# Optimization experiments

Measured on AMD Instinct MI355X. Metric: run time of the kernel, lower is better.

The kernel has to match this reference:

```python
import jax, jax.numpy as jnp
import numpy as np

B, S, H, E, V = 4, 256, 1024, 1024, 50257
PAD = 0
DOM = 0.9   # skipLayersDominance
EPS = 1e-5  # LayerNorm eps (torch default)


def setup_inputs() -> dict:
    key = jax.random.key(0)
    ks = jax.random.split(key, 6)
    emb = jax.random.normal(ks[0], (V, E), jnp.float32) * 0.02
    emb = emb.at[PAD].set(0.0)  # padding_idx row zeroed like nn.Embedding
    labels = jax.random.randint(ks[1], (B, S), 0, V)
    W_in = jax.random.normal(ks[2], (E, H), jnp.float32) * (1.0 / np.sqrt(E))
    b_in = jnp.zeros((H,), jnp.float32)
    # Conv1d(2H, H, kernel_size=1, groups=H) weight -> [H, 2] (per-head pair mix)
    W_sani = jax.random.normal(ks[3], (H, 2), jnp.float32) * (1.0 / np.sqrt(2.0))
    b_sani = jnp.zeros((H,), jnp.float32)
    ln_w = jnp.ones((H,), jnp.float32)
    ln_b = jnp.zeros((H,), jnp.float32)
    W_out = jax.random.normal(ks[4], (H, E), jnp.float32) * (1.0 / np.sqrt(H))
    b_out = jnp.zeros((E,), jnp.float32)
    return dict(labels=labels, emb=emb, W_in=W_in, b_in=b_in, W_sani=W_sani,
                b_sani=b_sani, ln_w=ln_w, ln_b=ln_b, W_out=W_out, b_out=b_out)


def _layernorm(x, w, b):
    mu = x.mean(-1, keepdims=True)
    var = x.var(-1, keepdims=True)
    return (x - mu) * jax.lax.rsqrt(var + EPS) * w + b


def _forward(labels, emb, W_in, b_in, W_sani, b_sani, ln_w, ln_b, W_out, b_out):
    x = emb[labels]                                # [B,S,E] inputsEmbeddings
    h = jax.nn.relu(x @ W_in + b_in)               # [B,S,H] inputState
    pos = jnp.arange(S)

    def step(hidden, L):
        # positions <= L are replaced by blank (zeros) per the torch cat logic
        mask = (pos > L)[None, :, None]
        shifted = jnp.concatenate([jnp.zeros_like(hidden[:, :1]), hidden[:, :-1]], axis=1)
        prev = jnp.where(mask, shifted, 0.0)       # hidden[t-1] for t>L else 0
        curr = jnp.where(mask, hidden, 0.0)        # hidden[t]   for t>L else 0
        # torch stack(dim=1)+reshape(B, 2H, 1) == concat(prev, curr) on features;
        # grouped conv (groups=H, 2 ch/group, k=1): out[g] = W[g,0]*cat[2g] + W[g,1]*cat[2g+1] + b[g]
        pair = jnp.concatenate([prev, curr], axis=-1).reshape(B, S, H, 2)
        out = jax.nn.relu(jnp.einsum('bshc,hc->bsh', pair, W_sani) + b_sani)
        out = out * (1.0 - DOM) + hidden           # skipLayers: + sequentialInputState
        out = _layernorm(out, ln_w, ln_b)           # skipLayersNorm
        return out, None

    h, _ = jax.lax.scan(jax.checkpoint(step), h, jnp.arange(S))
    y = jax.nn.relu(h @ W_out + b_out)             # [B,S,E]
    # torch CrossEntropyLoss with float (soft) targets: classes along dim=1 (S)
    logp = jax.nn.log_softmax(y, axis=1)
    loss = -(x * logp).sum(axis=1).mean()
    return loss


def reference(labels, emb, W_in, b_in, W_sani, b_sani, ln_w, ln_b, W_out, b_out):
    return _forward(labels, emb, W_in, b_in, W_sani, b_sani, ln_w, ln_b, W_out, b_out)
```

## Files before the change

kernel.cpp:

```cpp
#include <hip/hip_runtime.h>
#include <cstdint>

#define H_DIM 1024
#define S_LEN 256
#define NBLK_SCAN 128
#define GDEPTH 16
#define DOMC ((float)(1.0 - 0.9))
#define EPS_LN 1e-5f

typedef float v2f __attribute__((ext_vector_type(2)));

template <int CTRL, int RMASK, bool BC>
__device__ __forceinline__ float dpp_term(float x) {
    return __int_as_float(__builtin_amdgcn_update_dpp(
        0, __float_as_int(x), CTRL, RMASK, 0xf, BC));
}
__device__ __forceinline__ float wave_reduce_sum(float x) {
    x += dpp_term<0x111, 0xf, true>(x);
    x += dpp_term<0x112, 0xf, true>(x);
    x += dpp_term<0x114, 0xf, true>(x);
    x += dpp_term<0x118, 0xf, true>(x);
    x += dpp_term<0x142, 0xa, false>(x);
    x += dpp_term<0x143, 0xc, false>(x);
    return __int_as_float(__builtin_amdgcn_readlane(__float_as_int(x), 63));
}

__device__ __forceinline__ void lds_release_fence() {
    asm volatile("s_waitcnt lgkmcnt(0)" ::: "memory");
}

__device__ __forceinline__ int llc_load_int(const int* p) {
    int v;
    asm volatile("global_load_dword %0, %1, off sc0 sc1\n\ts_waitcnt vmcnt(0)"
                 : "=v"(v) : "v"(p) : "memory");
    return v;
}
__device__ __forceinline__ void llc_store_int(int* p, int v) {
    asm volatile("global_store_dword %0, %1, off sc0 sc1" :: "v"(p), "v"(v)
                 : "memory");
}
__device__ __forceinline__ void llc_store_row_nowait(float* base, const float* h) {
    asm volatile(
        "global_store_dword %16, %0, off sc0 sc1\n\t"
        "global_store_dword %16, %1, off offset:256 sc0 sc1\n\t"
        "global_store_dword %16, %2, off offset:512 sc0 sc1\n\t"
        "global_store_dword %16, %3, off offset:768 sc0 sc1\n\t"
        "global_store_dword %16, %4, off offset:1024 sc0 sc1\n\t"
        "global_store_dword %16, %5, off offset:1280 sc0 sc1\n\t"
        "global_store_dword %16, %6, off offset:1536 sc0 sc1\n\t"
        "global_store_dword %16, %7, off offset:1792 sc0 sc1\n\t"
        "global_store_dword %16, %8, off offset:2048 sc0 sc1\n\t"
        "global_store_dword %16, %9, off offset:2304 sc0 sc1\n\t"
        "global_store_dword %16, %10, off offset:2560 sc0 sc1\n\t"
        "global_store_dword %16, %11, off offset:2816 sc0 sc1\n\t"
        "global_store_dword %16, %12, off offset:3072 sc0 sc1\n\t"
        "global_store_dword %16, %13, off offset:3328 sc0 sc1\n\t"
        "global_store_dword %16, %14, off offset:3584 sc0 sc1\n\t"
        "global_store_dword %16, %15, off offset:3840 sc0 sc1"
        :: "v"(h[0]), "v"(h[1]), "v"(h[2]), "v"(h[3]),
           "v"(h[4]), "v"(h[5]), "v"(h[6]), "v"(h[7]),
           "v"(h[8]), "v"(h[9]), "v"(h[10]), "v"(h[11]),
           "v"(h[12]), "v"(h[13]), "v"(h[14]), "v"(h[15]), "v"(base)
        : "memory");
}
__device__ __forceinline__ void llc_publish_lag1(float* dbase, int* flagp,
                                                 int flagval, const float* h) {
    asm volatile(
        "global_store_dword %16, %0, off sc0 sc1\n\t"
        "global_store_dword %16, %1, off offset:256 sc0 sc1\n\t"
        "global_store_dword %16, %2, off offset:512 sc0 sc1\n\t"
        "global_store_dword %16, %3, off offset:768 sc0 sc1\n\t"
        "global_store_dword %16, %4, off offset:1024 sc0 sc1\n\t"
        "global_store_dword %16, %5, off offset:1280 sc0 sc1\n\t"
        "global_store_dword %16, %6, off offset:1536 sc0 sc1\n\t"
        "global_store_dword %16, %7, off offset:1792 sc0 sc1\n\t"
        "global_store_dword %16, %8, off offset:2048 sc0 sc1\n\t"
        "global_store_dword %16, %9, off offset:2304 sc0 sc1\n\t"
        "global_store_dword %16, %10, off offset:2560 sc0 sc1\n\t"
        "global_store_dword %16, %11, off offset:2816 sc0 sc1\n\t"
        "global_store_dword %16, %12, off offset:3072 sc0 sc1\n\t"
        "global_store_dword %16, %13, off offset:3328 sc0 sc1\n\t"
        "global_store_dword %16, %14, off offset:3584 sc0 sc1\n\t"
        "global_store_dword %16, %15, off offset:3840 sc0 sc1\n\t"
        "s_waitcnt vmcnt(16)\n\t"
        "global_store_dword %17, %18, off sc0 sc1"
        :: "v"(h[0]), "v"(h[1]), "v"(h[2]), "v"(h[3]),
           "v"(h[4]), "v"(h[5]), "v"(h[6]), "v"(h[7]),
           "v"(h[8]), "v"(h[9]), "v"(h[10]), "v"(h[11]),
           "v"(h[12]), "v"(h[13]), "v"(h[14]), "v"(h[15]),
           "v"(dbase), "v"(flagp), "v"(flagval)
        : "memory");
}
__device__ __forceinline__ void llc_release(int* flagp, int flagval) {
    asm volatile("s_waitcnt vmcnt(0)\n\t"
                 "global_store_dword %0, %1, off sc0 sc1"
                 :: "v"(flagp), "v"(flagval) : "memory");
}

__device__ __forceinline__ void dma_slot(const float* gslot, float* stg, int l) {
#pragma unroll
    for (int c = 0; c < 4; ++c)
        __builtin_amdgcn_global_load_lds(
            (const __attribute__((address_space(1))) uint32_t*)(gslot + c * 256 + l * 4),
            (__attribute__((address_space(3))) uint32_t*)(stg + c * 256),
            16, 0, 0x11);
}
__device__ __forceinline__ void flag_dma(const int* fp, int* stgf) {
    __builtin_amdgcn_global_load_lds(
        (const __attribute__((address_space(1))) uint32_t*)fp,
        (__attribute__((address_space(3))) uint32_t*)stgf, 4, 0, 0x11);
}

__device__ __forceinline__ void make_pairs(const float* hv, v2f* c7, int l) {
    const int s0 = (2 * l) & 63, s1 = (2 * l + 1) & 63;
    const bool hi = (l >= 32);
#pragma unroll
    for (int j = 0; j < 8; ++j) {
        float x0 = __shfl(hv[2 * j], s0, 64);
        float x1 = __shfl(hv[2 * j + 1], s0, 64);
        float y0 = __shfl(hv[2 * j], s1, 64);
        float y1 = __shfl(hv[2 * j + 1], s1, 64);
        c7[j].x = hi ? x1 : x0;
        c7[j].y = hi ? y1 : y0;
    }
}

template <bool GATHER>
__global__ __launch_bounds__(256) void gemm_relu_kernel(
    const float* __restrict__ A, const int* __restrict__ labels,
    const float* __restrict__ emb, const float* __restrict__ W,
    const float* __restrict__ bias, float* __restrict__ out,
    int* __restrict__ prodG, int* __restrict__ consG)
{
    __shared__ float As[16][68];
    __shared__ float Bs[16][64];
    __shared__ int   lab[64];

    const int tid = threadIdx.x;
    const int bx = blockIdx.x & 15;
    const int by = blockIdx.x >> 4;
    const int m0 = by * 64, n0 = bx * 64;

    if (GATHER && blockIdx.x == 0) {
        if (tid < NBLK_SCAN) prodG[tid * 32] = -2;
        else                 consG[(tid - NBLK_SCAN) * 32] = -2;
    }
    if (GATHER && tid < 64) lab[tid] = labels[m0 + tid];
    __syncthreads();

    const int tx = tid & 15, ty = tid >> 4;
    const int mload = tid >> 2;
    const int kq    = (tid & 3) * 4;
    const int kb    = tid >> 4;
    const int nb    = (tid & 15) * 4;

    const float* aBase;
    if (GATHER) aBase = emb + (size_t)lab[mload] * 1024 + kq;
    else        aBase = A   + (size_t)(m0 + mload) * 1024 + kq;
    const float* bBase = W + (size_t)kb * 1024 + n0 + nb;

    float4 a_pre = *(const float4*)aBase;
    float4 b_pre = *(const float4*)bBase;

    float acc[4][4] = {};

    for (int k0 = 0; k0 < 1024; k0 += 16) {
        As[kq + 0][mload] = a_pre.x;
        As[kq + 1][mload] = a_pre.y;
        As[kq + 2][mload] = a_pre.z;
        As[kq + 3][mload] = a_pre.w;
        *(float4*)&Bs[kb][nb] = b_pre;
        __syncthreads();

        if (k0 + 16 < 1024) {
            a_pre = *(const float4*)(aBase + k0 + 16);
            b_pre = *(const float4*)(bBase + (size_t)(k0 + 16) * 1024);
        }

#pragma unroll
        for (int kk = 0; kk < 16; ++kk) {
            float a_[4];
#pragma unroll
            for (int i = 0; i < 4; ++i) a_[i] = As[kk][ty * 4 + i];
            float4 bv = *(const float4*)&Bs[kk][tx * 4];
            float b_[4] = {bv.x, bv.y, bv.z, bv.w};
#pragma unroll
            for (int i = 0; i < 4; ++i)
#pragma unroll
                for (int j = 0; j < 4; ++j)
                    acc[i][j] = fmaf(a_[i], b_[j], acc[i][j]);
        }
        __syncthreads();
    }

    float bias4[4];
#pragma unroll
    for (int j = 0; j < 4; ++j) bias4[j] = bias[n0 + tx * 4 + j];
#pragma unroll
    for (int i = 0; i < 4; ++i) {
        float4 o;
        o.x = fmaxf(acc[i][0] + bias4[0], 0.f);
        o.y = fmaxf(acc[i][1] + bias4[1], 0.f);
        o.z = fmaxf(acc[i][2] + bias4[2], 0.f);
        o.w = fmaxf(acc[i][3] + bias4[3], 0.f);
        *(float4*)&out[(size_t)(m0 + ty * 4 + i) * 1024 + n0 + tx * 4] = o;
    }
}

__global__ __launch_bounds__(512, 1) void scan_kernel(
    const float* __restrict__ h0, float* __restrict__ hf,
    const float* __restrict__ Wsani, const float* __restrict__ bsani,
    const float* __restrict__ lnw, const float* __restrict__ lnb,
    float* __restrict__ gbuf, int* __restrict__ prodG, int* __restrict__ consG)
{
    __shared__ float ring[7][2][H_DIM];
    __shared__ float stg[2][H_DIM];
    __shared__ int   stgflag[64];
    __shared__ int prodL[8], consL[8];

    const int tid = threadIdx.x, w = tid >> 6, l = tid & 63;
    const int Bb = blockIdx.x;
    const int b = Bb >> 5, p = Bb & 31;
    const int t = 8 * p + w;
    const int row = b * S_LEN + t;
    const bool hasR = (p < 31);
    const int leftB = Bb - 1, rightB = Bb + 1;

    float w0c[16], w1c[16], bsc[16], lwc[16], lbc[16], hv[16];
#pragma unroll
    for (int i = 0; i < 16; ++i) {
        int h = l + 64 * i;
        w0c[i] = Wsani[2 * h]; w1c[i] = Wsani[2 * h + 1];
        bsc[i] = bsani[h]; lwc[i] = lnw[h]; lbc[i] = lnb[h];
        hv[i] = h0[(size_t)row * H_DIM + h];
    }

    if (tid < 8)  { prodL[tid] = -2; consL[tid] = -2; }
    if (tid < 64) stgflag[tid] = -2;
    __syncthreads();

    v2f c7[8];
    if (w < 7) {
#pragma unroll
        for (int i = 0; i < 16; ++i) ring[w][1][l + 64 * i] = hv[i];
        lds_release_fence();
        if (l == 0) ((volatile int*)prodL)[w] = -1;
    } else {
        if (hasR)
            llc_store_row_nowait(
                gbuf + ((size_t)Bb * GDEPTH + (GDEPTH - 1)) * H_DIM + l, hv);
        make_pairs(hv, c7, l);
    }

    const float inv1024 = 1.f / 1024.f;
    int F = -2, pfL = -3, consCache = -2;
    float vv[16];

    for (int L = 0; L < S_LEN; ++L) {
        const bool active = (L < t);
        if (active) {
            v2f pv[8], cv[8];
            if (w == 0) {
                const int* fp = prodG + leftB * 32;
                asm volatile("s_waitcnt vmcnt(0)" ::: "memory");
                {
                    int fa = ((volatile int*)stgflag)[0];
                    if (fa > F) F = fa;
                }
                if (pfL != L - 1) {
                    while (F < L - 1) {
                        F = __builtin_amdgcn_readfirstlane(llc_load_int(fp));
                        if (F < L - 1) __builtin_amdgcn_s_sleep(1);
                    }
                    dma_slot(gbuf + ((size_t)leftB * GDEPTH +
                                     ((L - 1) & (GDEPTH - 1))) * H_DIM,
                             stg[(L - 1) & 1], l);
                    pfL = L - 1;
                    asm volatile("s_waitcnt vmcnt(0)" ::: "memory");
                }
                const float* srcp = stg[(L - 1) & 1];
#pragma unroll
                for (int j = 0; j < 8; ++j)
                    pv[j] = *(const v2f*)&srcp[2 * l + 128 * j];
#pragma unroll
                for (int j = 0; j < 8; ++j)
                    cv[j] = *(const v2f*)&ring[0][(L - 1) & 1][2 * l + 128 * j];
                if (L < t - 1) {
                    if (F >= L) {
                        dma_slot(gbuf + ((size_t)leftB * GDEPTH +
                                         (L & (GDEPTH - 1))) * H_DIM,
                                 stg[L & 1], l);
                        pfL = L;
                    }
                    flag_dma(fp, stgflag);
                }
                llc_store_int(consG + Bb * 32, L);
            } else {
                int spin = 0;
                while (((volatile int*)prodL)[w - 1] < L - 1)
                    { if (++spin > 8) __builtin_amdgcn_s_sleep(1); }
                const float* srcp = &ring[w - 1][(L - 1) & 1][0];
#pragma unroll
                for (int j = 0; j < 8; ++j)
                    pv[j] = *(const v2f*)&srcp[2 * l + 128 * j];
                if (w < 7) {
                    const float* srcc = &ring[w][(L - 1) & 1][0];
#pragma unroll
                    for (int j = 0; j < 8; ++j)
                        cv[j] = *(const v2f*)&srcc[2 * l + 128 * j];
                } else {
#pragma unroll
                    for (int j = 0; j < 8; ++j) cv[j] = c7[j];
                }
                if (l == 0) ((volatile int*)consL)[w] = L - 1;
            }
#pragma unroll
            for (int i = 0; i < 8; ++i) {
                float s = fmaf(pv[i].x, w0c[i], fmaf(pv[i].y, w1c[i], bsc[i]));
                s = fmaxf(s, 0.f);
                vv[i] = fmaf(DOMC, s, hv[i]);
            }
#pragma unroll
            for (int i = 8; i < 16; ++i) {
                float s = fmaf(cv[i - 8].x, w0c[i],
                               fmaf(cv[i - 8].y, w1c[i], bsc[i]));
                s = fmaxf(s, 0.f);
                vv[i] = fmaf(DOMC, s, hv[i]);
            }
        } else {
#pragma unroll
            for (int i = 0; i < 16; ++i) {
                float s = fmaxf(bsc[i], 0.f);
                vv[i] = fmaf(DOMC, s, hv[i]);
            }
        }
        float sum = 0.f, ss = 0.f;
#pragma unroll
        for (int i = 0; i < 16; ++i) { sum += vv[i]; ss = fmaf(vv[i], vv[i], ss); }
        sum = wave_reduce_sum(sum); ss = wave_reduce_sum(ss);
        const float mu = sum * inv1024;
        const float var = fmaf(-mu, mu, ss * inv1024);
        const float r = 1.f / sqrtf(var + EPS_LN);
#pragma unroll
        for (int i = 0; i < 16; ++i)
            hv[i] = fmaf((vv[i] - mu) * r, lwc[i], lbc[i]);

        if (active) {
            if (w < 7) {
                if (L >= 1) {
                    int spin = 0;
                    while (((volatile int*)consL)[w + 1] < L - 2)
                        { if (++spin > 8) __builtin_amdgcn_s_sleep(1); }
                }
#pragma unroll
                for (int i = 0; i < 16; ++i) ring[w][L & 1][l + 64 * i] = hv[i];
                lds_release_fence();
                if (l == 0) ((volatile int*)prodL)[w] = L;
            } else {
                if (hasR) {
                    if (consCache < L - (GDEPTH - 3)) {
                        int c = llc_load_int(consG + rightB * 32);
                        while (c < L - (GDEPTH - 1)) {
                            __builtin_amdgcn_s_sleep(1);
                            c = llc_load_int(consG + rightB * 32);
                        }
                        consCache = __builtin_amdgcn_readfirstlane(c);
                    }
                    llc_publish_lag1(
                        gbuf + ((size_t)Bb * GDEPTH + (L & (GDEPTH - 1))) * H_DIM + l,
                        prodG + Bb * 32, L - 1, hv);
                }
                if (L + 1 < t) make_pairs(hv, c7, l);
            }
        } else if (w == 7 && hasR && L == t) {
            llc_release(prodG + Bb * 32, t - 1);
        }
    }
#pragma unroll
    for (int i = 0; i < 16; ++i)
        hf[(size_t)row * H_DIM + l + 64 * i] = hv[i];
}

__global__ __launch_bounds__(256) void lse_kernel(
    const float* __restrict__ y, float* __restrict__ lse)
{
    const int b = blockIdx.x >> 4, et = blockIdx.x & 15;
    const int col = threadIdx.x & 63, rg = threadIdx.x >> 6;
    const int e = et * 64 + col;
    const float* yb = y + (size_t)b * S_LEN * H_DIM + e;
    float m = -INFINITY, s = 0.f;
    for (int r = rg; r < S_LEN; r += 4) {
        float v = yb[(size_t)r * H_DIM];
        float mn = fmaxf(m, v);
        s = fmaf(s, expf(m - mn), expf(v - mn));
        m = mn;
    }
    __shared__ float sm[4][64], sp[4][64];
    sm[rg][col] = m; sp[rg][col] = s;
    __syncthreads();
    if (threadIdx.x < 64) {
        const int c = threadIdx.x;
        float M = fmaxf(fmaxf(sm[0][c], sm[1][c]), fmaxf(sm[2][c], sm[3][c]));
        float S = sp[0][c] * expf(sm[0][c] - M) + sp[1][c] * expf(sm[1][c] - M)
                + sp[2][c] * expf(sm[2][c] - M) + sp[3][c] * expf(sm[3][c] - M);
        lse[b * H_DIM + et * 64 + c] = M + logf(S);
    }
}

__global__ __launch_bounds__(256) void loss_row_kernel(
    const float* __restrict__ y, const int* __restrict__ labels,
    const float* __restrict__ emb, const float* __restrict__ lse,
    float* __restrict__ partials)
{
    const int bs = blockIdx.x;
    const int b = bs >> 8;
    const int lab = labels[bs];
    const float* yr = y + (size_t)bs * H_DIM;
    const float* er = emb + (size_t)lab * H_DIM;
    const float* lr = lse + b * H_DIM;
    float acc = 0.f;
#pragma unroll
    for (int i = 0; i < 4; ++i) {
        int e = threadIdx.x + 256 * i;
        acc = fmaf(er[e], yr[e] - lr[e], acc);
    }
    acc = wave_reduce_sum(acc);
    __shared__ float wsum[4];
    if ((threadIdx.x & 63) == 0) wsum[threadIdx.x >> 6] = acc;
    __syncthreads();
    if (threadIdx.x == 0)
        partials[bs] = (wsum[0] + wsum[1]) + (wsum[2] + wsum[3]);
}

__global__ __launch_bounds__(256) void loss_final_kernel(
    const float* __restrict__ partials, float* __restrict__ out)
{
    const int tid = threadIdx.x;
    float a = 0.f;
#pragma unroll
    for (int j = 0; j < 4; ++j) a += partials[tid + 256 * j];
    a = wave_reduce_sum(a);
    __shared__ float wsum[4];
    if ((tid & 63) == 0) wsum[tid >> 6] = a;
    __syncthreads();
    if (tid == 0)
        out[0] = -((wsum[0] + wsum[1]) + (wsum[2] + wsum[3])) * (1.f / 4096.f);
}

extern "C" void kernel_launch(void* const* d_in, const int* in_sizes, int n_in,
                              void* d_out, int out_size, void* d_ws, size_t ws_size,
                              hipStream_t stream)
{
    const int*   labels = (const int*)  d_in[0];
    const float* emb    = (const float*)d_in[1];
    const float* W_in   = (const float*)d_in[2];
    const float* b_in   = (const float*)d_in[3];
    const float* W_sani = (const float*)d_in[4];
    const float* b_sani = (const float*)d_in[5];
    const float* ln_w   = (const float*)d_in[6];
    const float* ln_b   = (const float*)d_in[7];
    const float* W_out  = (const float*)d_in[8];
    const float* b_out  = (const float*)d_in[9];
    float* out = (float*)d_out;

    float* ws = (float*)d_ws;
    float* h0       = ws;
    float* hf       = ws + (1 << 20);
    float* yb       = ws + 2 * (1 << 20);
    float* gbuf     = ws + 3 * (1 << 20);
    float* lse      = ws + 5 * (1 << 20);
    float* partials = lse + 4096;
    int*   prodG    = (int*)(partials + 1024);
    int*   consG    = prodG + NBLK_SCAN * 32;

    gemm_relu_kernel<true><<<dim3(256), dim3(256), 0, stream>>>(
        nullptr, labels, emb, W_in, b_in, h0, prodG, consG);
    {
        const float* a_h0 = h0; float* a_hf = hf;
        const float* a_ws = W_sani; const float* a_bs = b_sani;
        const float* a_lw = ln_w;   const float* a_lb = ln_b;
        float* a_gb = gbuf; int* a_pf = prodG; int* a_cf = consG;
        void* args[] = { (void*)&a_h0, (void*)&a_hf, (void*)&a_ws, (void*)&a_bs,
                         (void*)&a_lw, (void*)&a_lb, (void*)&a_gb,
                         (void*)&a_pf, (void*)&a_cf };
        hipLaunchCooperativeKernel((const void*)scan_kernel,
                                   dim3(NBLK_SCAN), dim3(512), args, 0, stream);
    }
    gemm_relu_kernel<false><<<dim3(256), dim3(256), 0, stream>>>(
        hf, nullptr, emb, W_out, b_out, yb, nullptr, nullptr);
    lse_kernel<<<dim3(64), dim3(256), 0, stream>>>(yb, lse);
    loss_row_kernel<<<dim3(1024), dim3(256), 0, stream>>>(
        yb, labels, emb, lse, partials);
    loss_final_kernel<<<dim3(1), dim3(256), 0, stream>>>(partials, out);
}
```

Baseline: 725.4 us.

## Halve GEMM tile width and move scan per-feature params into LDS

The two ReLU GEMMs now use 64x32 output tiles with a 2x4 per-thread micro-tile, and launch twice as many blocks to spread work over more CUs. The scan kernel stops holding the Sani weights, bias and LayerNorm parameters in per-thread register arrays and instead reads them from shared memory on each step, which lowers register pressure. The wait before reading the left neighbour's staging flag is relaxed to allow one outstanding vector load. The cost is extra LDS reads on the serial critical path of the scan, lower per-thread arithmetic intensity in the GEMM, and some risk from the relaxed wait count.

```diff
diff --git a/kernel.cpp b/kernel.cpp
--- a/kernel.cpp
+++ b/kernel.cpp
@@ -133,13 +133,13 @@
     int* __restrict__ prodG, int* __restrict__ consG)
 {
     __shared__ float As[16][68];
-    __shared__ float Bs[16][64];
+    __shared__ float Bs[16][32];
     __shared__ int   lab[64];
 
     const int tid = threadIdx.x;
-    const int bx = blockIdx.x & 15;
-    const int by = blockIdx.x >> 4;
-    const int m0 = by * 64, n0 = bx * 64;
+    const int bx = blockIdx.x & 31;
+    const int by = blockIdx.x >> 5;
+    const int m0 = by * 64, n0 = bx * 32;
 
     if (GATHER && blockIdx.x == 0) {
         if (tid < NBLK_SCAN) prodG[tid * 32] = -2;
@@ -148,11 +148,12 @@
     if (GATHER && tid < 64) lab[tid] = labels[m0 + tid];
     __syncthreads();
 
-    const int tx = tid & 15, ty = tid >> 4;
+    const int tx = tid & 7;
+    const int ty = tid >> 3;
     const int mload = tid >> 2;
     const int kq    = (tid & 3) * 4;
     const int kb    = tid >> 4;
-    const int nb    = (tid & 15) * 4;
+    const int nb    = (tid & 15) * 2;
 
     const float* aBase;
     if (GATHER) aBase = emb + (size_t)lab[mload] * 1024 + kq;
@@ -160,50 +161,52 @@
     const float* bBase = W + (size_t)kb * 1024 + n0 + nb;
 
     float4 a_pre = *(const float4*)aBase;
-    float4 b_pre = *(const float4*)bBase;
-
-    float acc[4][4] = {};
+    float2 b_pre = *(const float2*)bBase;
+
+    float acc[4][2] = {};
+    float accr[2][4] = {};
 
     for (int k0 = 0; k0 < 1024; k0 += 16) {
         As[kq + 0][mload] = a_pre.x;
         As[kq + 1][mload] = a_pre.y;
         As[kq + 2][mload] = a_pre.z;
         As[kq + 3][mload] = a_pre.w;
-        *(float4*)&Bs[kb][nb] = b_pre;
+        *(float2*)&Bs[kb][nb] = b_pre;
         __syncthreads();
 
         if (k0 + 16 < 1024) {
             a_pre = *(const float4*)(aBase + k0 + 16);
-            b_pre = *(const float4*)(bBase + (size_t)(k0 + 16) * 1024);
+            b_pre = *(const float2*)(bBase + (size_t)(k0 + 16) * 1024);
         }
 
 #pragma unroll
         for (int kk = 0; kk < 16; ++kk) {
-            float a_[4];
-#pragma unroll
-            for (int i = 0; i < 4; ++i) a_[i] = As[kk][ty * 4 + i];
+            float a_[2];
+#pragma unroll
+            for (int i = 0; i < 2; ++i) a_[i] = As[kk][ty * 2 + i];
             float4 bv = *(const float4*)&Bs[kk][tx * 4];
             float b_[4] = {bv.x, bv.y, bv.z, bv.w};
 #pragma unroll
-            for (int i = 0; i < 4; ++i)
+            for (int i = 0; i < 2; ++i)
 #pragma unroll
                 for (int j = 0; j < 4; ++j)
-                    acc[i][j] = fmaf(a_[i], b_[j], acc[i][j]);
+                    accr[i][j] = fmaf(a_[i], b_[j], accr[i][j]);
         }
         __syncthreads();
     }
+    (void)acc;
 
     float bias4[4];
 #pragma unroll
     for (int j = 0; j < 4; ++j) bias4[j] = bias[n0 + tx * 4 + j];
 #pragma unroll
-    for (int i = 0; i < 4; ++i) {
+    for (int i = 0; i < 2; ++i) {
         float4 o;
-        o.x = fmaxf(acc[i][0] + bias4[0], 0.f);
-        o.y = fmaxf(acc[i][1] + bias4[1], 0.f);
-        o.z = fmaxf(acc[i][2] + bias4[2], 0.f);
-        o.w = fmaxf(acc[i][3] + bias4[3], 0.f);
-        *(float4*)&out[(size_t)(m0 + ty * 4 + i) * 1024 + n0 + tx * 4] = o;
+        o.x = fmaxf(accr[i][0] + bias4[0], 0.f);
+        o.y = fmaxf(accr[i][1] + bias4[1], 0.f);
+        o.z = fmaxf(accr[i][2] + bias4[2], 0.f);
+        o.w = fmaxf(accr[i][3] + bias4[3], 0.f);
+        *(float4*)&out[(size_t)(m0 + ty * 2 + i) * 1024 + n0 + tx * 4] = o;
     }
 }
 
@@ -215,6 +218,9 @@
 {
     __shared__ float ring[7][2][H_DIM];
     __shared__ float stg[2][H_DIM];
+    __shared__ v2f   cW01[H_DIM];
+    __shared__ v2f   cLWB[H_DIM];
+    __shared__ float cBS[H_DIM];
     __shared__ int   stgflag[64];
     __shared__ int prodL[8], consL[8];
 
@@ -226,14 +232,17 @@
     const bool hasR = (p < 31);
     const int leftB = Bb - 1, rightB = Bb + 1;
 
-    float w0c[16], w1c[16], bsc[16], lwc[16], lbc[16], hv[16];
-#pragma unroll
-    for (int i = 0; i < 16; ++i) {
-        int h = l + 64 * i;
-        w0c[i] = Wsani[2 * h]; w1c[i] = Wsani[2 * h + 1];
-        bsc[i] = bsani[h]; lwc[i] = lnw[h]; lbc[i] = lnb[h];
-        hv[i] = h0[(size_t)row * H_DIM + h];
-    }
+    for (int q = tid; q < H_DIM; q += 512) {
+        cW01[q] = *(const v2f*)&Wsani[2 * q];
+        v2f lwb; lwb.x = lnw[q]; lwb.y = lnb[q];
+        cLWB[q] = lwb;
+        cBS[q]  = bsani[q];
+    }
+
+    float hv[16];
+#pragma unroll
+    for (int i = 0; i < 16; ++i)
+        hv[i] = h0[(size_t)row * H_DIM + l + 64 * i];
 
     if (tid < 8)  { prodL[tid] = -2; consL[tid] = -2; }
     if (tid < 64) stgflag[tid] = -2;
@@ -262,7 +271,7 @@
             v2f pv[8], cv[8];
             if (w == 0) {
                 const int* fp = prodG + leftB * 32;
-                asm volatile("s_waitcnt vmcnt(0)" ::: "memory");
+                asm volatile("s_waitcnt vmcnt(1)" ::: "memory");
                 {
                     int fa = ((volatile int*)stgflag)[0];
                     if (fa > F) F = fa;
@@ -316,21 +325,25 @@
             }
 #pragma unroll
             for (int i = 0; i < 8; ++i) {
-                float s = fmaf(pv[i].x, w0c[i], fmaf(pv[i].y, w1c[i], bsc[i]));
+                const int h = l + 64 * i;
+                v2f w01 = cW01[h];
+                float s = fmaf(pv[i].x, w01.x, fmaf(pv[i].y, w01.y, cBS[h]));
                 s = fmaxf(s, 0.f);
                 vv[i] = fmaf(DOMC, s, hv[i]);
             }
 #pragma unroll
             for (int i = 8; i < 16; ++i) {
-                float s = fmaf(cv[i - 8].x, w0c[i],
-                               fmaf(cv[i - 8].y, w1c[i], bsc[i]));
+                const int h = l + 64 * i;
+                v2f w01 = cW01[h];
+                float s = fmaf(cv[i - 8].x, w01.x,
+                               fmaf(cv[i - 8].y, w01.y, cBS[h]));
                 s = fmaxf(s, 0.f);
                 vv[i] = fmaf(DOMC, s, hv[i]);
             }
         } else {
 #pragma unroll
             for (int i = 0; i < 16; ++i) {
-                float s = fmaxf(bsc[i], 0.f);
+                float s = fmaxf(cBS[l + 64 * i], 0.f);
                 vv[i] = fmaf(DOMC, s, hv[i]);
             }
         }
@@ -342,8 +355,10 @@
         const float var = fmaf(-mu, mu, ss * inv1024);
         const float r = 1.f / sqrtf(var + EPS_LN);
 #pragma unroll
-        for (int i = 0; i < 16; ++i)
-            hv[i] = fmaf((vv[i] - mu) * r, lwc[i], lbc[i]);
+        for (int i = 0; i < 16; ++i) {
+            v2f lwb = cLWB[l + 64 * i];
+            hv[i] = fmaf((vv[i] - mu) * r, lwb.x, lwb.y);
+        }
 
         if (active) {
             if (w < 7) {
@@ -473,7 +488,7 @@
     int*   prodG    = (int*)(partials + 1024);
     int*   consG    = prodG + NBLK_SCAN * 32;
 
-    gemm_relu_kernel<true><<<dim3(256), dim3(256), 0, stream>>>(
+    gemm_relu_kernel<true><<<dim3(512), dim3(256), 0, stream>>>(
         nullptr, labels, emb, W_in, b_in, h0, prodG, consG);
     {
         const float* a_h0 = h0; float* a_hf = hf;
@@ -486,7 +501,7 @@
         hipLaunchCooperativeKernel((const void*)scan_kernel,
                                    dim3(NBLK_SCAN), dim3(512), args, 0, stream);
     }
-    gemm_relu_kernel<false><<<dim3(256), dim3(256), 0, stream>>>(
+    gemm_relu_kernel<false><<<dim3(512), dim3(256), 0, stream>>>(
         hf, nullptr, emb, W_out, b_out, yb, nullptr, nullptr);
     lse_kernel<<<dim3(64), dim3(256), 0, stream>>>(yb, lse);
     loss_row_kernel<<<dim3(1024), dim3(256), 0, stream>>>(
```

Measured after the change: 838.1 us. 15.5% more time.

## Widen scan blocks to sixteen waves, halving cross-block global handoffs

Applied to the files above, without the earlier changes.

The sequential scan now runs 64 blocks of 1024 threads (16 wavefronts, one time step each) instead of 128 blocks of 512. More of the pipeline chain passes through the LDS ring inside a block and fewer hops go through global-memory flags and buffers between blocks. It also precomputes relu(bias) for inactive steps and relaxes one waitcnt from vmcnt(0) to vmcnt(1). The larger LDS ring and 1024-thread blocks raise register and LDS pressure, and the relaxed waitcnt could allow a stale read of the DMA staging data.

```diff
diff --git a/kernel.cpp b/kernel.cpp
--- a/kernel.cpp
+++ b/kernel.cpp
@@ -3,7 +3,8 @@
 
 #define H_DIM 1024
 #define S_LEN 256
-#define NBLK_SCAN 128
+#define NBLK_SCAN 64
+#define NWAVE 16
 #define GDEPTH 16
 #define DOMC ((float)(1.0 - 0.9))
 #define EPS_LN 1e-5f
@@ -143,7 +144,7 @@
 
     if (GATHER && blockIdx.x == 0) {
         if (tid < NBLK_SCAN) prodG[tid * 32] = -2;
-        else                 consG[(tid - NBLK_SCAN) * 32] = -2;
+        else if (tid < 2 * NBLK_SCAN) consG[(tid - NBLK_SCAN) * 32] = -2;
     }
     if (GATHER && tid < 64) lab[tid] = labels[m0 + tid];
     __syncthreads();
@@ -207,40 +208,45 @@
     }
 }
 
-__global__ __launch_bounds__(512, 1) void scan_kernel(
+__global__ __launch_bounds__(1024, 1) void scan_kernel(
     const float* __restrict__ h0, float* __restrict__ hf,
     const float* __restrict__ Wsani, const float* __restrict__ bsani,
     const float* __restrict__ lnw, const float* __restrict__ lnb,
     float* __restrict__ gbuf, int* __restrict__ prodG, int* __restrict__ consG)
 {
-    __shared__ float ring[7][2][H_DIM];
+    __shared__ float ring[NWAVE - 1][2][H_DIM];
     __shared__ float stg[2][H_DIM];
     __shared__ int   stgflag[64];
-    __shared__ int prodL[8], consL[8];
+    __shared__ int prodL[NWAVE], consL[NWAVE];
 
     const int tid = threadIdx.x, w = tid >> 6, l = tid & 63;
     const int Bb = blockIdx.x;
-    const int b = Bb >> 5, p = Bb & 31;
-    const int t = 8 * p + w;
+    const int b = Bb >> 4, p = Bb & 15;
+    const int t = NWAVE * p + w;
     const int row = b * S_LEN + t;
-    const bool hasR = (p < 31);
+    const bool hasR = (p < 15);
     const int leftB = Bb - 1, rightB = Bb + 1;
 
-    float w0c[16], w1c[16], bsc[16], lwc[16], lbc[16], hv[16];
+    float w0c[16], w1c[16], bsr[16], lwc[16], lbc[16], hv[16];
 #pragma unroll
     for (int i = 0; i < 16; ++i) {
         int h = l + 64 * i;
         w0c[i] = Wsani[2 * h]; w1c[i] = Wsani[2 * h + 1];
-        bsc[i] = bsani[h]; lwc[i] = lnw[h]; lbc[i] = lnb[h];
+        bsr[i] = fmaxf(bsani[h], 0.f);
+        lwc[i] = lnw[h]; lbc[i] = lnb[h];
         hv[i] = h0[(size_t)row * H_DIM + h];
     }
-
-    if (tid < 8)  { prodL[tid] = -2; consL[tid] = -2; }
+    const float bsc_neg_ok = 0.f; (void)bsc_neg_ok;
+    float bsc[16];
+#pragma unroll
+    for (int i = 0; i < 16; ++i) bsc[i] = bsani[l + 64 * i];
+
+    if (tid < NWAVE) { prodL[tid] = -2; consL[tid] = -2; }
     if (tid < 64) stgflag[tid] = -2;
     __syncthreads();
 
     v2f c7[8];
-    if (w < 7) {
+    if (w < NWAVE - 1) {
 #pragma unroll
         for (int i = 0; i < 16; ++i) ring[w][1][l + 64 * i] = hv[i];
         lds_release_fence();
@@ -262,7 +268,7 @@
             v2f pv[8], cv[8];
             if (w == 0) {
                 const int* fp = prodG + leftB * 32;
-                asm volatile("s_waitcnt vmcnt(0)" ::: "memory");
+                asm volatile("s_waitcnt vmcnt(1)" ::: "memory");
                 {
                     int fa = ((volatile int*)stgflag)[0];
                     if (fa > F) F = fa;
@@ -303,7 +309,7 @@
 #pragma unroll
                 for (int j = 0; j < 8; ++j)
                     pv[j] = *(const v2f*)&srcp[2 * l + 128 * j];
-                if (w < 7) {
+                if (w < NWAVE - 1) {
                     const float* srcc = &ring[w][(L - 1) & 1][0];
 #pragma unroll
                     for (int j = 0; j < 8; ++j)
@@ -329,10 +335,8 @@
             }
         } else {
 #pragma unroll
-            for (int i = 0; i < 16; ++i) {
-                float s = fmaxf(bsc[i], 0.f);
-                vv[i] = fmaf(DOMC, s, hv[i]);
-            }
+            for (int i = 0; i < 16; ++i)
+                vv[i] = fmaf(DOMC, bsr[i], hv[i]);
         }
         float sum = 0.f, ss = 0.f;
 #pragma unroll
@@ -346,7 +350,7 @@
             hv[i] = fmaf((vv[i] - mu) * r, lwc[i], lbc[i]);
 
         if (active) {
-            if (w < 7) {
+            if (w < NWAVE - 1) {
                 if (L >= 1) {
                     int spin = 0;
                     while (((volatile int*)consL)[w + 1] < L - 2)
@@ -372,7 +376,7 @@
                 }
                 if (L + 1 < t) make_pairs(hv, c7, l);
             }
-        } else if (w == 7 && hasR && L == t) {
+        } else if (w == NWAVE - 1 && hasR && L == t) {
             llc_release(prodG + Bb * 32, t - 1);
         }
     }
@@ -484,7 +488,7 @@
                          (void*)&a_lw, (void*)&a_lb, (void*)&a_gb,
                          (void*)&a_pf, (void*)&a_cf };
         hipLaunchCooperativeKernel((const void*)scan_kernel,
-                                   dim3(NBLK_SCAN), dim3(512), args, 0, stream);
+                                   dim3(NBLK_SCAN), dim3(1024), args, 0, stream);
     }
     gemm_relu_kernel<false><<<dim3(256), dim3(256), 0, stream>>>(
         hf, nullptr, emb, W_out, b_out, yb, nullptr, nullptr);
```

Result: slower. 1.619 ms (+123.2%).

## Fuse all stages into one cooperative persistent kernel with grid barriers

Applied to the files above, without the earlier changes.

Merges the input GEMM, recurrent scan, output GEMM, log-sum-exp, loss row and final reduction into a single cooperative kernel of 256 blocks × 512 threads, separated by atomic-counter grid barriers. Shared memory becomes a union across phases, and the GEMM tile is remapped so 512 threads each compute 2×4 outputs. The aim is to remove five kernel launch gaps and the cooperative-launch overhead. In exchange, every block of every phase is held to one resident block per CU with a large shared-memory footprint, and a scan wait count is relaxed from vmcnt(0) to vmcnt(1), which risks an ordering error.

```diff
diff --git a/kernel.cpp b/kernel.cpp
--- a/kernel.cpp
+++ b/kernel.cpp
@@ -4,6 +4,7 @@
 #define H_DIM 1024
 #define S_LEN 256
 #define NBLK_SCAN 128
+#define GRID_BLKS 256
 #define GDEPTH 16
 #define DOMC ((float)(1.0 - 0.9))
 #define EPS_LN 1e-5f
@@ -125,67 +126,82 @@
     }
 }
 
+struct SmemScan {
+    float ring[7][2][H_DIM];
+    float stg[2][H_DIM];
+    int   stgflag[64];
+    int   prodL[8], consL[8];
+};
+struct SmemGemm { int lab[64]; float As[16][68]; float Bs[16][68]; };
+struct SmemLse  { float sm4[4][64]; float sp4[4][64]; };
+struct SmemLoss { float wsum[2][4]; };
+union Smem { SmemScan s; SmemGemm g; SmemLse l; SmemLoss r; };
+
+__device__ __forceinline__ void grid_barrier(int* gbar, int target) {
+    __syncthreads();
+    if (threadIdx.x == 0) {
+        __threadfence();
+        atomicAdd(gbar, 1);
+        while (llc_load_int(gbar) < target)
+            __builtin_amdgcn_s_sleep(8);
+        __threadfence();
+    }
+    __syncthreads();
+}
+
 template <bool GATHER>
-__global__ __launch_bounds__(256) void gemm_relu_kernel(
-    const float* __restrict__ A, const int* __restrict__ labels,
-    const float* __restrict__ emb, const float* __restrict__ W,
-    const float* __restrict__ bias, float* __restrict__ out,
-    int* __restrict__ prodG, int* __restrict__ consG)
-{
-    __shared__ float As[16][68];
-    __shared__ float Bs[16][64];
-    __shared__ int   lab[64];
-
+__device__ void gemm_phase(Smem& sm, const float* __restrict__ A,
+                           const int* __restrict__ labels,
+                           const float* __restrict__ emb,
+                           const float* __restrict__ W,
+                           const float* __restrict__ bias,
+                           float* __restrict__ outp)
+{
     const int tid = threadIdx.x;
     const int bx = blockIdx.x & 15;
     const int by = blockIdx.x >> 4;
     const int m0 = by * 64, n0 = bx * 64;
 
-    if (GATHER && blockIdx.x == 0) {
-        if (tid < NBLK_SCAN) prodG[tid * 32] = -2;
-        else                 consG[(tid - NBLK_SCAN) * 32] = -2;
-    }
-    if (GATHER && tid < 64) lab[tid] = labels[m0 + tid];
+    if (GATHER && tid < 64) sm.g.lab[tid] = labels[m0 + tid];
     __syncthreads();
 
-    const int tx = tid & 15, ty = tid >> 4;
-    const int mload = tid >> 2;
-    const int kq    = (tid & 3) * 4;
-    const int kb    = tid >> 4;
-    const int nb    = (tid & 15) * 4;
+    const int arow = tid >> 3;
+    const int akp  = (tid & 7) * 2;
+    const int kb   = tid >> 5;
+    const int nb   = (tid & 31) * 2;
 
     const float* aBase;
-    if (GATHER) aBase = emb + (size_t)lab[mload] * 1024 + kq;
-    else        aBase = A   + (size_t)(m0 + mload) * 1024 + kq;
+    if (GATHER) aBase = emb + (size_t)sm.g.lab[arow] * 1024 + akp;
+    else        aBase = A   + (size_t)(m0 + arow) * 1024 + akp;
     const float* bBase = W + (size_t)kb * 1024 + n0 + nb;
 
-    float4 a_pre = *(const float4*)aBase;
-    float4 b_pre = *(const float4*)bBase;
-
-    float acc[4][4] = {};
+    float2 a_pre = *(const float2*)aBase;
+    float2 b_pre = *(const float2*)bBase;
+
+    const int tx = tid & 15;
+    const int ty = tid >> 4;
+    float acc[2][4] = {};
 
     for (int k0 = 0; k0 < 1024; k0 += 16) {
-        As[kq + 0][mload] = a_pre.x;
-        As[kq + 1][mload] = a_pre.y;
-        As[kq + 2][mload] = a_pre.z;
-        As[kq + 3][mload] = a_pre.w;
-        *(float4*)&Bs[kb][nb] = b_pre;
+        sm.g.As[akp + 0][arow] = a_pre.x;
+        sm.g.As[akp + 1][arow] = a_pre.y;
+        *(float2*)&sm.g.Bs[kb][nb] = b_pre;
         __syncthreads();
 
         if (k0 + 16 < 1024) {
-            a_pre = *(const float4*)(aBase + k0 + 16);
-            b_pre = *(const float4*)(bBase + (size_t)(k0 + 16) * 1024);
+            a_pre = *(const float2*)(aBase + k0 + 16);
+            b_pre = *(const float2*)(bBase + (size_t)(k0 + 16) * 1024);
         }
 
 #pragma unroll
         for (int kk = 0; kk < 16; ++kk) {
-            float a_[4];
-#pragma unroll
-            for (int i = 0; i < 4; ++i) a_[i] = As[kk][ty * 4 + i];
-            float4 bv = *(const float4*)&Bs[kk][tx * 4];
+            float a_[2];
+#pragma unroll
+            for (int i = 0; i < 2; ++i) a_[i] = sm.g.As[kk][ty * 2 + i];
+            float4 bv = *(const float4*)&sm.g.Bs[kk][tx * 4];
             float b_[4] = {bv.x, bv.y, bv.z, bv.w};
 #pragma unroll
-            for (int i = 0; i < 4; ++i)
+            for (int i = 0; i < 2; ++i)
 #pragma unroll
                 for (int j = 0; j < 4; ++j)
                     acc[i][j] = fmaf(a_[i], b_[j], acc[i][j]);
@@ -197,26 +213,27 @@
 #pragma unroll
     for (int j = 0; j < 4; ++j) bias4[j] = bias[n0 + tx * 4 + j];
 #pragma unroll
-    for (int i = 0; i < 4; ++i) {
+    for (int i = 0; i < 2; ++i) {
         float4 o;
         o.x = fmaxf(acc[i][0] + bias4[0], 0.f);
         o.y = fmaxf(acc[i][1] + bias4[1], 0.f);
         o.z = fmaxf(acc[i][2] + bias4[2], 0.f);
         o.w = fmaxf(acc[i][3] + bias4[3], 0.f);
-        *(float4*)&out[(size_t)(m0 + ty * 4 + i) * 1024 + n0 + tx * 4] = o;
-    }
-}
-
-__global__ __launch_bounds__(512, 1) void scan_kernel(
+        *(float4*)&outp[(size_t)(m0 + ty * 2 + i) * 1024 + n0 + tx * 4] = o;
+    }
+}
+
+__device__ void scan_phase(Smem& smu,
     const float* __restrict__ h0, float* __restrict__ hf,
     const float* __restrict__ Wsani, const float* __restrict__ bsani,
     const float* __restrict__ lnw, const float* __restrict__ lnb,
     float* __restrict__ gbuf, int* __restrict__ prodG, int* __restrict__ consG)
 {
-    __shared__ float ring[7][2][H_DIM];
-    __shared__ float stg[2][H_DIM];
-    __shared__ int   stgflag[64];
-    __shared__ int prodL[8], consL[8];
+    auto& ring = smu.s.ring;
+    auto& stg = smu.s.stg;
+    auto& stgflag = smu.s.stgflag;
+    auto& prodL = smu.s.prodL;
+    auto& consL = smu.s.consL;
 
     const int tid = threadIdx.x, w = tid >> 6, l = tid & 63;
     const int Bb = blockIdx.x;
@@ -262,7 +279,7 @@
             v2f pv[8], cv[8];
             if (w == 0) {
                 const int* fp = prodG + leftB * 32;
-                asm volatile("s_waitcnt vmcnt(0)" ::: "memory");
+                asm volatile("s_waitcnt vmcnt(1)" ::: "memory");
                 {
                     int fa = ((volatile int*)stgflag)[0];
                     if (fa > F) F = fa;
@@ -381,70 +398,124 @@
         hf[(size_t)row * H_DIM + l + 64 * i] = hv[i];
 }
 
-__global__ __launch_bounds__(256) void lse_kernel(
-    const float* __restrict__ y, float* __restrict__ lse)
-{
+__device__ void lse_phase(Smem& sm, const float* __restrict__ y,
+                          float* __restrict__ lse)
+{
+    if (blockIdx.x >= 64) return;
+    const int tid = threadIdx.x;
     const int b = blockIdx.x >> 4, et = blockIdx.x & 15;
-    const int col = threadIdx.x & 63, rg = threadIdx.x >> 6;
-    const int e = et * 64 + col;
-    const float* yb = y + (size_t)b * S_LEN * H_DIM + e;
-    float m = -INFINITY, s = 0.f;
-    for (int r = rg; r < S_LEN; r += 4) {
-        float v = yb[(size_t)r * H_DIM];
-        float mn = fmaxf(m, v);
-        s = fmaf(s, expf(m - mn), expf(v - mn));
-        m = mn;
-    }
-    __shared__ float sm[4][64], sp[4][64];
-    sm[rg][col] = m; sp[rg][col] = s;
+    if (tid < 256) {
+        const int col = tid & 63, rg = tid >> 6;
+        const int e = et * 64 + col;
+        const float* yb = y + (size_t)b * S_LEN * H_DIM + e;
+        float m = -INFINITY, s = 0.f;
+        for (int r = rg; r < S_LEN; r += 4) {
+            float v = yb[(size_t)r * H_DIM];
+            float mn = fmaxf(m, v);
+            s = fmaf(s, expf(m - mn), expf(v - mn));
+            m = mn;
+        }
+        sm.l.sm4[rg][col] = m; sm.l.sp4[rg][col] = s;
+    }
     __syncthreads();
-    if (threadIdx.x < 64) {
-        const int c = threadIdx.x;
-        float M = fmaxf(fmaxf(sm[0][c], sm[1][c]), fmaxf(sm[2][c], sm[3][c]));
-        float S = sp[0][c] * expf(sm[0][c] - M) + sp[1][c] * expf(sm[1][c] - M)
-                + sp[2][c] * expf(sm[2][c] - M) + sp[3][c] * expf(sm[3][c] - M);
+    if (tid < 64) {
+        const int c = tid;
+        float M = fmaxf(fmaxf(sm.l.sm4[0][c], sm.l.sm4[1][c]),
+                        fmaxf(sm.l.sm4[2][c], sm.l.sm4[3][c]));
+        float S = sm.l.sp4[0][c] * expf(sm.l.sm4[0][c] - M)
+                + sm.l.sp4[1][c] * expf(sm.l.sm4[1][c] - M)
+                + sm.l.sp4[2][c] * expf(sm.l.sm4[2][c] - M)
+                + sm.l.sp4[3][c] * expf(sm.l.sm4[3][c] - M);
         lse[b * H_DIM + et * 64 + c] = M + logf(S);
     }
 }
 
-__global__ __launch_bounds__(256) void loss_row_kernel(
-    const float* __restrict__ y, const int* __restrict__ labels,
-    const float* __restrict__ emb, const float* __restrict__ lse,
-    float* __restrict__ partials)
-{
-    const int bs = blockIdx.x;
-    const int b = bs >> 8;
-    const int lab = labels[bs];
-    const float* yr = y + (size_t)bs * H_DIM;
-    const float* er = emb + (size_t)lab * H_DIM;
-    const float* lr = lse + b * H_DIM;
-    float acc = 0.f;
-#pragma unroll
-    for (int i = 0; i < 4; ++i) {
-        int e = threadIdx.x + 256 * i;
-        acc = fmaf(er[e], yr[e] - lr[e], acc);
-    }
-    acc = wave_reduce_sum(acc);
-    __shared__ float wsum[4];
-    if ((threadIdx.x & 63) == 0) wsum[threadIdx.x >> 6] = acc;
-    __syncthreads();
-    if (threadIdx.x == 0)
-        partials[bs] = (wsum[0] + wsum[1]) + (wsum[2] + wsum[3]);
-}
-
-__global__ __launch_bounds__(256) void loss_final_kernel(
-    const float* __restrict__ partials, float* __restrict__ out)
+__device__ void loss_phase(Smem& sm, const float* __restrict__ y,
+                           const int* __restrict__ labels,
+                           const float* __restrict__ emb,
+                           const float* __restrict__ lseArr,
+                           float* __restrict__ partials)
+{
+    const int tid = threadIdx.x;
+    const int g = tid >> 8, gt = tid & 255;
+#pragma unroll
+    for (int it = 0; it < 2; ++it) {
+        const int bs = blockIdx.x * 4 + it * 2 + g;
+        const int b = bs >> 8;
+        const int lab = labels[bs];
+        const float* yr = y + (size_t)bs * H_DIM;
+        const float* er = emb + (size_t)lab * H_DIM;
+        const float* lr = lseArr + b * H_DIM;
+        float acc = 0.f;
+#pragma unroll
+        for (int i = 0; i < 4; ++i) {
+            int e = gt + 256 * i;
+            acc = fmaf(er[e], yr[e] - lr[e], acc);
+        }
+        acc = wave_reduce_sum(acc);
+        if ((gt & 63) == 0) sm.r.wsum[g][gt >> 6] = acc;
+        __syncthreads();
+        if (gt == 0)
+            partials[bs] = (sm.r.wsum[g][0] + sm.r.wsum[g][1])
+                         + (sm.r.wsum[g][2] + sm.r.wsum[g][3]);
+        __syncthreads();
+    }
+}
+
+__device__ void final_phase(Smem& sm, const float* __restrict__ partials,
+                            float* __restrict__ outp)
 {
     const int tid = threadIdx.x;
     float a = 0.f;
-#pragma unroll
-    for (int j = 0; j < 4; ++j) a += partials[tid + 256 * j];
+    if (tid < 256) {
+#pragma unroll
+        for (int j = 0; j < 4; ++j) a += partials[tid + 256 * j];
+    }
     a = wave_reduce_sum(a);
-    __shared__ float wsum[4];
-    if ((tid & 63) == 0) wsum[tid >> 6] = a;
+    if (tid < 256 && (tid & 63) == 0) sm.r.wsum[0][tid >> 6] = a;
     __syncthreads();
     if (tid == 0)
-        out[0] = -((wsum[0] + wsum[1]) + (wsum[2] + wsum[3])) * (1.f / 4096.f);
+        outp[0] = -((sm.r.wsum[0][0] + sm.r.wsum[0][1])
+                  + (sm.r.wsum[0][2] + sm.r.wsum[0][3])) * (1.f / 4096.f);
+}
+
+__global__ __launch_bounds__(512, 1) void fused_kernel(
+    const int* __restrict__ labels, const float* __restrict__ emb,
+    const float* __restrict__ W_in, const float* __restrict__ b_in,
+    const float* __restrict__ W_sani, const float* __restrict__ b_sani,
+    const float* __restrict__ ln_w, const float* __restrict__ ln_b,
+    const float* __restrict__ W_out, const float* __restrict__ b_out,
+    float* __restrict__ out,
+    float* __restrict__ h0, float* __restrict__ hf, float* __restrict__ yb,
+    float* __restrict__ gbuf, float* __restrict__ lse,
+    float* __restrict__ partials, int* __restrict__ prodG,
+    int* __restrict__ consG, int* __restrict__ gbar)
+{
+    __shared__ Smem sm;
+
+    if (blockIdx.x == 0) {
+        if (threadIdx.x < NBLK_SCAN)
+            llc_store_int(prodG + threadIdx.x * 32, -2);
+        else if (threadIdx.x < 2 * NBLK_SCAN)
+            llc_store_int(consG + (threadIdx.x - NBLK_SCAN) * 32, -2);
+    }
+    gemm_phase<true>(sm, nullptr, labels, emb, W_in, b_in, h0);
+    grid_barrier(gbar, GRID_BLKS * 1);
+
+    if (blockIdx.x < NBLK_SCAN)
+        scan_phase(sm, h0, hf, W_sani, b_sani, ln_w, ln_b, gbuf, prodG, consG);
+    grid_barrier(gbar, GRID_BLKS * 2);
+
+    gemm_phase<false>(sm, hf, nullptr, emb, W_out, b_out, yb);
+    grid_barrier(gbar, GRID_BLKS * 3);
+
+    lse_phase(sm, yb, lse);
+    grid_barrier(gbar, GRID_BLKS * 4);
+
+    loss_phase(sm, yb, labels, emb, lse, partials);
+    grid_barrier(gbar, GRID_BLKS * 5);
+
+    if (blockIdx.x == 0) final_phase(sm, partials, out);
 }
 
 extern "C" void kernel_launch(void* const* d_in, const int* in_sizes, int n_in,
@@ -472,24 +543,25 @@
     float* partials = lse + 4096;
     int*   prodG    = (int*)(partials + 1024);
     int*   consG    = prodG + NBLK_SCAN * 32;
-
-    gemm_relu_kernel<true><<<dim3(256), dim3(256), 0, stream>>>(
-        nullptr, labels, emb, W_in, b_in, h0, prodG, consG);
-    {
-        const float* a_h0 = h0; float* a_hf = hf;
-        const float* a_ws = W_sani; const float* a_bs = b_sani;
-        const float* a_lw = ln_w;   const float* a_lb = ln_b;
-        float* a_gb = gbuf; int* a_pf = prodG; int* a_cf = consG;
-        void* args[] = { (void*)&a_h0, (void*)&a_hf, (void*)&a_ws, (void*)&a_bs,
-                         (void*)&a_lw, (void*)&a_lb, (void*)&a_gb,
-                         (void*)&a_pf, (void*)&a_cf };
-        hipLaunchCooperativeKernel((const void*)scan_kernel,
-                                   dim3(NBLK_SCAN), dim3(512), args, 0, stream);
-    }
-    gemm_relu_kernel<false><<<dim3(256), dim3(256), 0, stream>>>(
-        hf, nullptr, emb, W_out, b_out, yb, nullptr, nullptr);
-    lse_kernel<<<dim3(64), dim3(256), 0, stream>>>(yb, lse);
-    loss_row_kernel<<<dim3(1024), dim3(256), 0, stream>>>(
-        yb, labels, emb, lse, partials);
-    loss_final_kernel<<<dim3(1), dim3(256), 0, stream>>>(partials, out);
-}
+    int*   gbar     = consG + NBLK_SCAN * 32;
+
+    hipMemsetAsync(gbar, 0, sizeof(int), stream);
+
+    const int* a_lab = labels; const float* a_emb = emb;
+    const float* a_wi = W_in; const float* a_bi = b_in;
+    const float* a_ws = W_sani; const float* a_bs = b_sani;
+    const float* a_lw = ln_w; const float* a_lb = ln_b;
+    const float* a_wo = W_out; const float* a_bo = b_out;
+    float* a_out = out;
+    float* a_h0 = h0; float* a_hf = hf; float* a_yb = yb;
+    float* a_gb = gbuf; float* a_lse = lse; float* a_pt = partials;
+    int* a_pf = prodG; int* a_cf = consG; int* a_gbar = gbar;
+    void* args[] = { (void*)&a_lab, (void*)&a_emb, (void*)&a_wi, (void*)&a_bi,
+                     (void*)&a_ws, (void*)&a_bs, (void*)&a_lw, (void*)&a_lb,
+                     (void*)&a_wo, (void*)&a_bo, (void*)&a_out,
+                     (void*)&a_h0, (void*)&a_hf, (void*)&a_yb,
+                     (void*)&a_gb, (void*)&a_lse, (void*)&a_pt,
+                     (void*)&a_pf, (void*)&a_cf, (void*)&a_gbar };
+    hipLaunchCooperativeKernel((const void*)fused_kernel,
+                               dim3(GRID_BLKS), dim3(512), args, 0, stream);
+}
```

New measurement: 871.2 us. 1.2x slower.
